# Kernel tuning notes

Measured on AMD Instinct MI355X. Metric: run time of the kernel, lower is better.

Reference implementation:

```python
import jax, jax.numpy as jnp
import numpy as np

B, S, D, H, DFF = 4, 2048, 1024, 16, 4096
DK = D // H  # = d_v
NEG = -1e30  # stands in for float('-inf'); fully-masked rows zeroed explicitly


def setup_inputs() -> dict:
    key = jax.random.key(0)
    ks = jax.random.split(key, 12)
    scale = lambda fan_in: fan_in ** -0.5
    # padding mask: positions >= random length are padded (True = pad)
    lens = jax.random.randint(ks[0], (B,), S // 2, S + 1)
    src_padding_mask = jnp.arange(S)[None, :] >= lens[:, None]
    return {
        "src": jax.random.normal(ks[1], (B, S, D), jnp.float32),
        "src_padding_mask": src_padding_mask,
        # per-head projections, stored as [H, D, DK] (x @ W, i.e. torch W.T)
        "Wq": jax.random.normal(ks[2], (H, D, DK), jnp.float32) * scale(D),
        "Wk": jax.random.normal(ks[3], (H, D, DK), jnp.float32) * scale(D),
        "Wv": jax.random.normal(ks[4], (H, D, DK), jnp.float32) * scale(D),
        "Wo": jax.random.normal(ks[5], (D, D), jnp.float32) * scale(D),
        "g1": jnp.ones((D,), jnp.float32),
        "g2": jnp.ones((D,), jnp.float32),
        "W1": jax.random.normal(ks[6], (D, DFF), jnp.float32) * scale(D),
        "V1": jax.random.normal(ks[7], (D, DFF), jnp.float32) * scale(D),
        "W2": jax.random.normal(ks[8], (DFF, D), jnp.float32) * scale(DFF),
    }


def _rmsnorm(x, gamma):
    # rms = sqrt(sum(x^2)/size); out = gamma * x / rms
    rms = jnp.sqrt(jnp.sum(x * x, axis=-1, keepdims=True) / x.shape[-1])
    return gamma * x / rms


def _encoder_layer(src, pad_mask, Wq, Wk, Wv, Wo, g1, g2, W1, V1, W2):
    x = _rmsnorm(src, g1)
    # all heads at once: q,k,v -> [B,H,S,DK]
    q = jnp.einsum('bsd,hdk->bhsk', x, Wq)
    k = jnp.einsum('bsd,hdk->bhsk', x, Wk)
    v = jnp.einsum('bsd,hdk->bhsk', x, Wv)
    scores = jnp.einsum('bhsk,bhtk->bhst', q, k) * (DK ** -0.5)  # [B,H,S,S]
    mask = pad_mask[:, None, :, None] | pad_mask[:, None, None, :]
    scores = jnp.where(mask, NEG, scores)
    attn = jax.nn.softmax(scores, axis=-1)
    # torch: fully -inf rows softmax to nan -> nan_to_num(0). Zero padded query rows.
    attn = jnp.where(pad_mask[:, None, :, None], 0.0, attn)
    o = jnp.einsum('bhst,bhtk->bhsk', attn, v)            # [B,H,S,DK]
    o = o.transpose(0, 2, 1, 3).reshape(src.shape[0], src.shape[1], -1)  # concat heads
    sa = src + o @ Wo
    y = _rmsnorm(sa, g2)
    ff = (jax.nn.silu(y @ W1) * (y @ V1)) @ W2
    return sa + ff


def reference(src, src_padding_mask, Wq, Wk, Wv, Wo, g1, g2, W1, V1, W2):
    return _encoder_layer(src, src_padding_mask, Wq, Wk, Wv, Wo, g1, g2, W1, V1, W2)
```

## Files before the change

kernel.cpp:

```cpp
#include <hip/hip_runtime.h>
#include <hip/hip_bf16.h>

typedef short short8 __attribute__((ext_vector_type(8)));
typedef float f32x4 __attribute__((ext_vector_type(4)));
typedef float f32x16 __attribute__((ext_vector_type(16)));
typedef unsigned short u16;
typedef unsigned short u16x4 __attribute__((ext_vector_type(4)));

__device__ __forceinline__ u16 f2bf(float f) {
  __hip_bfloat16 h = __float2bfloat16(f);
  return __builtin_bit_cast(u16, h);
}
__device__ __forceinline__ float bf2f(u16 u) {
  return __bfloat162float(__builtin_bit_cast(__hip_bfloat16, u));
}
__device__ __forceinline__ void gload_lds16(const void* g, void* l) {
  __builtin_amdgcn_global_load_lds(
      (const __attribute__((address_space(1))) void*)g,
      (__attribute__((address_space(3))) void*)l, 16, 0, 0);
}
__device__ __forceinline__ unsigned cvtpk(float lo, float hi) {
  unsigned r;
  asm("v_cvt_pk_bf16_f32 %0, %1, %2" : "=v"(r) : "v"(lo), "v"(hi));
  return r;
}

__global__ void compute_lens(const unsigned char* __restrict__ mask, int* __restrict__ lens) {
  __shared__ int flag;
  __shared__ int cnt[4];
  const int tid = threadIdx.x;
  if (tid == 0) flag = 0;
  if (tid < 4) cnt[tid] = 0;
  __syncthreads();
  int found = 0;
  for (int i = tid; i < 8192; i += 256)
    if (mask[i] == 1 && (i & 3) != 0) found = 1;
  if (found) atomicOr(&flag, 1);
  __syncthreads();
  int l0 = 0, l1 = 0, l2 = 0, l3 = 0;
  if (flag) {
    for (int i = tid; i < 8192; i += 256) {
      int z = (mask[i] == 0);
      int b = i >> 11;
      l0 += z & (b == 0); l1 += z & (b == 1); l2 += z & (b == 2); l3 += z & (b == 3);
    }
  } else {
    const int* mi = (const int*)mask;
    for (int i = tid; i < 8192; i += 256) {
      int z = (mi[i] == 0);
      int b = i >> 11;
      l0 += z & (b == 0); l1 += z & (b == 1); l2 += z & (b == 2); l3 += z & (b == 3);
    }
  }
  if (l0) atomicAdd(&cnt[0], l0);
  if (l1) atomicAdd(&cnt[1], l1);
  if (l2) atomicAdd(&cnt[2], l2);
  if (l3) atomicAdd(&cnt[3], l3);
  __syncthreads();
  if (tid < 4) lens[tid] = cnt[tid];
}

__global__ void convT_all(const float* __restrict__ Wq, const float* __restrict__ Wk,
                          const float* __restrict__ Wv, const float* __restrict__ Wo,
                          const float* __restrict__ W1, const float* __restrict__ V1,
                          const float* __restrict__ W2,
                          u16* __restrict__ WqkvT, u16* __restrict__ WoT,
                          u16* __restrict__ W1V1T, u16* __restrict__ W2T) {
  __shared__ float t[32][33];
  int b = (int)blockIdx.x;
  const float* in;
  u16* op;
  int K, N, n0, k0, ilv = 0;
  if (b < 3072) {
    const int which = b >> 10;
    b &= 1023;
    in = (which == 0) ? Wq : (which == 1) ? Wk : Wv;
    const int z = b >> 6;
    in += (size_t)z * 65536;
    op = WqkvT + (size_t)which * 1048576 + (size_t)z * 65536;
    K = 1024; N = 64;
    n0 = (b & 1) * 32; k0 = ((b >> 1) & 31) * 32;
  } else if (b < 4096) {
    b -= 3072;
    in = Wo; op = WoT; K = 1024; N = 1024;
    n0 = (b & 31) * 32; k0 = (b >> 5) * 32;
  } else if (b < 12288) {
    const int which = (b - 4096) >> 12;
    b = (b - 4096) & 4095;
    in = which ? V1 : W1; op = W1V1T; K = 1024; N = 4096; ilv = 1 + which;
    n0 = (b & 127) * 32; k0 = (b >> 7) * 32;
  } else {
    b -= 12288;
    in = W2; op = W2T; K = 4096; N = 1024;
    n0 = (b & 31) * 32; k0 = (b >> 5) * 32;
  }
  const int tx = threadIdx.x & 31, ty = threadIdx.x >> 5;
  for (int i = ty; i < 32; i += 8)
    t[i][tx] = in[(size_t)(k0 + i) * N + n0 + tx];
  __syncthreads();
  for (int i = ty; i < 32; i += 8) {
    const int rn = n0 + i;
    const int r = ilv ? ((((rn >> 4) << 5) | (rn & 15)) | ((ilv - 1) << 4)) : rn;
    op[(size_t)r * K + k0 + tx] = f2bf(t[tx][i]);
  }
}

__global__ void rmsnorm_kernel(const float* __restrict__ in, const float* __restrict__ g,
                               u16* __restrict__ out) {
  __shared__ float psum[4];
  const int row = blockIdx.x, tid = threadIdx.x;
  const float4 x = ((const float4*)(in + (size_t)row * 1024))[tid];
  float ss = x.x * x.x + x.y * x.y + x.z * x.z + x.w * x.w;
  for (int m = 1; m < 64; m <<= 1) ss += __shfl_xor(ss, m, 64);
  if ((tid & 63) == 0) psum[tid >> 6] = ss;
  __syncthreads();
  const float tot = psum[0] + psum[1] + psum[2] + psum[3];
  const float inv = rsqrtf(tot * (1.0f / 1024.0f));
  const float4 gv = ((const float4*)g)[tid];
  u16x4 o;
  o[0] = f2bf(gv.x * x.x * inv); o[1] = f2bf(gv.y * x.y * inv);
  o[2] = f2bf(gv.z * x.z * inv); o[3] = f2bf(gv.w * x.w * inv);
  *(u16x4*)&out[(size_t)row * 1024 + tid * 4] = o;
}

enum { MQKV = 0, MSA = 1, MFSILU = 2, MFF2 = 3 };

template <int MODE, int BM>
__global__ __launch_bounds__(512, (BM == 64) ? 4 : 2) void gemm3(
    const u16* __restrict__ A, const u16* __restrict__ Bt,
    const int K,
    u16* __restrict__ oq, u16* __restrict__ ok, u16* __restrict__ ov,
    float* __restrict__ of, const float* __restrict__ afp,
    u16* __restrict__ ob) {
  constexpr int ABUF = BM * 64;
  constexpr bool P4 = (BM == 256);
  constexpr int MR = BM / 32;
  constexpr int AIT = BM / 64;
  constexpr int AFR = (MR < 4) ? MR : 4;
  __shared__ u16 lds[2 * ABUF + 32768];
  const int tid = threadIdx.x;
  const int w = tid >> 6, l = tid & 63;
  const int wr = w >> 2, wc = w & 3;
  const int lane16 = l & 15, lgrp = l >> 4;

  const int bid = (int)blockIdx.x, xcd = bid & 7, seq = bid >> 3;
  int by, bx;
  if (MODE == MQKV) {
    const int j = seq / 24, t5 = seq % 24;
    by = (xcd >> 2) * 32 + j * 8 + t5 / 3;
    bx = (xcd & 3) * 3 + t5 % 3;
  } else if (MODE == MFSILU) {
    by = (seq >> 5) * 8 + ((seq & 31) >> 2);
    bx = xcd * 4 + (seq & 3);
  } else {
    by = (xcd >> 1) * 32 + (seq >> 1);
    bx = (xcd & 1) * 2 + (seq & 1);
  }
  const int row0 = by * BM, col0 = bx * 256;

  auto stageA = [&](int kt, int buf) {
#pragma unroll
    for (int i = 0; i < AIT; ++i) {
      const int cc = i * 512 + tid;
      const int r = cc >> 3, j = (cc & 7) ^ (r & 7);
      gload_lds16(A + (size_t)(row0 + r) * K + kt * 64 + j * 8,
                  &lds[buf * ABUF + cc * 8]);
    }
  };
  auto stageB = [&](int kt, int buf) {
#pragma unroll
    for (int i = 0; i < 4; ++i) {
      const int cc = i * 512 + tid;
      const int r = cc >> 3, j = (cc & 7) ^ (r & 7);
      gload_lds16(Bt + (size_t)(col0 + r) * K + kt * 64 + j * 8,
                  &lds[2 * ABUF + buf * 16384 + cc * 8]);
    }
  };
  auto frofs = [&](int rrow, int ks) {
    return rrow * 64 + ((((ks << 2) + lgrp) ^ (rrow & 7)) << 3);
  };

  f32x4 zero = {0.f, 0.f, 0.f, 0.f};
  f32x4 acc[MR][4];
#pragma unroll
  for (int i = 0; i < MR; ++i)
#pragma unroll
    for (int j = 0; j < 4; ++j) acc[i][j] = zero;

  const int nkt = K >> 6;
  stageA(0, 0); stageB(0, 0); stageA(1, 1);
  if (P4) stageB(1, 1);

  for (int t = 0; t < nkt; ++t) {
    const int c = t & 1;
    if (t == nkt - 1)       asm volatile("s_waitcnt vmcnt(0)\ns_barrier" ::: "memory");
    else if (P4)            asm volatile("s_waitcnt vmcnt(8)\ns_barrier" ::: "memory");
    else if (AIT == 2)      asm volatile("s_waitcnt vmcnt(2)\ns_barrier" ::: "memory");
    else                    asm volatile("s_waitcnt vmcnt(1)\ns_barrier" ::: "memory");
    const u16* ap = &lds[c * ABUF];
    const u16* bp = &lds[2 * ABUF + c * 16384];
    short8 a[AFR][2], b01[2][2], b23[2][2];

    if (!P4) { if (t + 1 < nkt) stageB(t + 1, c ^ 1); }
#pragma unroll
    for (int mi = 0; mi < AFR; ++mi)
#pragma unroll
      for (int ks = 0; ks < 2; ++ks)
        a[mi][ks] = *(const short8*)&ap[frofs(wr * (BM / 2) + mi * 16 + lane16, ks)];
#pragma unroll
    for (int ni = 0; ni < 2; ++ni)
#pragma unroll
      for (int ks = 0; ks < 2; ++ks) {
        b01[ni][ks] = *(const short8*)&bp[frofs(wc * 64 + ni * 16 + lane16, ks)];
        b23[ni][ks] = *(const short8*)&bp[frofs(wc * 64 + (ni + 2) * 16 + lane16, ks)];
      }
    __builtin_amdgcn_s_setprio(1);
#pragma unroll
    for (int ks = 0; ks < 2; ++ks)
#pragma unroll
      for (int mi = 0; mi < AFR; ++mi)
#pragma unroll
        for (int ni = 0; ni < 2; ++ni)
          acc[mi][ni] = __builtin_amdgcn_mfma_f32_16x16x32_bf16(a[mi][ks], b01[ni][ks], acc[mi][ni], 0, 0, 0);
    __builtin_amdgcn_s_setprio(0);
    asm volatile("s_barrier" ::: "memory");

    if (P4) {
      __builtin_amdgcn_s_setprio(1);
#pragma unroll
      for (int ks = 0; ks < 2; ++ks)
#pragma unroll
        for (int mi = 0; mi < 4; ++mi)
#pragma unroll
          for (int ni = 0; ni < 2; ++ni)
            acc[mi][ni + 2] = __builtin_amdgcn_mfma_f32_16x16x32_bf16(a[mi][ks], b23[ni][ks], acc[mi][ni + 2], 0, 0, 0);
      __builtin_amdgcn_s_setprio(0);
#pragma unroll
      for (int mi = 0; mi < 4; ++mi)
#pragma unroll
        for (int ks = 0; ks < 2; ++ks)
          a[mi][ks] = *(const short8*)&ap[frofs(wr * 128 + (mi + 4) * 16 + lane16, ks)];
      asm volatile("s_barrier" ::: "memory");

      if (t + 2 < nkt) stageB(t + 2, c);
      __builtin_amdgcn_s_setprio(1);
#pragma unroll
      for (int ks = 0; ks < 2; ++ks)
#pragma unroll
        for (int mi = 0; mi < 4; ++mi)
#pragma unroll
          for (int ni = 0; ni < 2; ++ni)
            acc[(MR == 8 ? mi + 4 : mi)][ni] = __builtin_amdgcn_mfma_f32_16x16x32_bf16(a[mi][ks], b01[ni][ks], acc[(MR == 8 ? mi + 4 : mi)][ni], 0, 0, 0);
      __builtin_amdgcn_s_setprio(0);
      asm volatile("s_barrier" ::: "memory");

      if (t + 2 < nkt) stageA(t + 2, c);
      __builtin_amdgcn_s_setprio(1);
#pragma unroll
      for (int ks = 0; ks < 2; ++ks)
#pragma unroll
        for (int mi = 0; mi < 4; ++mi)
#pragma unroll
          for (int ni = 0; ni < 2; ++ni)
            acc[(MR == 8 ? mi + 4 : mi)][ni + 2] = __builtin_amdgcn_mfma_f32_16x16x32_bf16(a[mi][ks], b23[ni][ks], acc[(MR == 8 ? mi + 4 : mi)][ni + 2], 0, 0, 0);
      __builtin_amdgcn_s_setprio(0);
    } else {
      if (t + 2 < nkt) stageA(t + 2, c);
      __builtin_amdgcn_s_setprio(1);
#pragma unroll
      for (int ks = 0; ks < 2; ++ks)
#pragma unroll
        for (int mi = 0; mi < AFR; ++mi)
#pragma unroll
          for (int ni = 0; ni < 2; ++ni)
            acc[mi][ni + 2] = __builtin_amdgcn_mfma_f32_16x16x32_bf16(a[mi][ks], b23[ni][ks], acc[mi][ni + 2], 0, 0, 0);
      __builtin_amdgcn_s_setprio(0);
    }
  }
  asm volatile("s_barrier" ::: "memory");

  if (MODE == MQKV) {
#pragma unroll
    for (int mi = 0; mi < MR; ++mi) {
      const int sbase = row0 + wr * (BM / 2) + mi * 16 + lgrp * 4;
      const int bbt = sbase >> 11, sr = sbase & 2047;
#pragma unroll
      for (int ni = 0; ni < 4; ++ni) {
        const int j = col0 + wc * 64 + ni * 16 + lane16;
        const int which = j >> 10, rr = j & 1023, h = rr >> 6, kk = rr & 63;
        const int bh = bbt * 16 + h;
        if (which == 2) {
          u16x4 pk;
#pragma unroll
          for (int r = 0; r < 4; ++r) pk[r] = f2bf(acc[mi][ni][r]);
          *(u16x4*)&ov[((size_t)bh * 64 + kk) * 2048 + sr] = pk;
        } else {
          u16* dst = (which == 0) ? oq : ok;
          const float scl = (which == 0) ? 0.125f : 1.0f;
#pragma unroll
          for (int r = 0; r < 4; ++r)
            dst[((size_t)bh * 2048 + sr + r) * 64 + kk] = f2bf(acc[mi][ni][r] * scl);
        }
      }
    }
  } else if (MODE == MFSILU) {
    u16* ep = &lds[w * 576];
    const int orow = l >> 2, ocol = (l & 3) * 8;
#pragma unroll
    for (int mi = 0; mi < MR; ++mi) {
#pragma unroll
      for (int p = 0; p < 2; ++p)
#pragma unroll
        for (int r = 0; r < 4; ++r) {
          const float h1 = acc[mi][2 * p][r], h2 = acc[mi][2 * p + 1][r];
          ep[(lgrp * 4 + r) * 34 + p * 16 + lane16] = f2bf(h1 / (1.0f + __expf(-h1)) * h2);
        }
      short8 v = *(const short8*)&ep[orow * 34 + ocol];
      *(short8*)&ob[(size_t)(row0 + wr * (BM / 2) + mi * 16 + orow) * 4096 +
                    (col0 >> 1) + wc * 32 + ocol] = v;
    }
  } else {
#pragma unroll
    for (int mi = 0; mi < MR; ++mi) {
      const int row = row0 + wr * (BM / 2) + mi * 16 + lgrp * 4;
#pragma unroll
      for (int ni = 0; ni < 4; ++ni) {
        const int j = col0 + wc * 64 + ni * 16 + lane16;
#pragma unroll
        for (int r = 0; r < 4; ++r) {
          const size_t idx = (size_t)(row + r) * 1024 + j;
          const float base = (MODE == MSA) ? afp[idx] : of[idx];
          of[idx] = base + acc[mi][ni][r];
        }
      }
    }
  }
}

__global__ void attn2_kernel(const u16* __restrict__ qb, const u16* __restrict__ kb,
                             const u16* __restrict__ vT, u16* __restrict__ obuf,
                             const int* __restrict__ lens) {
  __shared__ u16 sm[9216];
  const int tid = threadIdx.x;
  const int l = tid & 63, wid = tid >> 6;
  const int l31 = l & 31, hi = l >> 5;
  const int bh = blockIdx.x, b = bh >> 4, h = bh & 15;
  const int q0 = blockIdx.y * 128;
  const int len = lens[b];

  if (q0 >= len) {
    short8 z = {0, 0, 0, 0, 0, 0, 0, 0};
#pragma unroll
    for (int c = 0; c < 4; ++c) {
      const int ck = c * 256 + tid;
      const int r = ck >> 3, j = ck & 7;
      *(short8*)&obuf[((size_t)b * 2048 + q0 + r) * 1024 + h * 64 + j * 8] = z;
    }
    return;
  }

  const int q0w = q0 + wid * 32;
  const u16* qp = qb + ((size_t)bh * 2048 + q0w + l31) * 64;
  short8 qf0 = *(const short8*)(qp + hi * 8);
  short8 qf1 = *(const short8*)(qp + 16 + hi * 8);
  short8 qf2 = *(const short8*)(qp + 32 + hi * 8);
  short8 qf3 = *(const short8*)(qp + 48 + hi * 8);

  f32x16 oa0 = {0.f,0.f,0.f,0.f,0.f,0.f,0.f,0.f,0.f,0.f,0.f,0.f,0.f,0.f,0.f,0.f};
  f32x16 oa1 = oa0;
  float m_run = -1e30f, l_run = 0.f;

  const int swz = (l31 & 7) << 3;
  const int nt = (len + 63) >> 6;
  for (int kt = 0; kt < nt; ++kt) {
    const int t0 = kt * 64;
    __syncthreads();
#pragma unroll
    for (int c = 0; c < 2; ++c) {
      const int ck = c * 256 + wid * 64 + l;
      const int r = ck >> 3;
      const int j = (ck & 7) ^ (r & 7);
      gload_lds16(kb + ((size_t)bh * 2048 + t0 + r) * 64 + j * 8,
                  &sm[(c * 256 + wid * 64) * 8]);
      gload_lds16(vT + ((size_t)bh * 64 + r) * 2048 + t0 + j * 8,
                  &sm[4096 + (c * 256 + wid * 64) * 8]);
    }
    __syncthreads();

    f32x16 sc0 = {0.f,0.f,0.f,0.f,0.f,0.f,0.f,0.f,0.f,0.f,0.f,0.f,0.f,0.f,0.f,0.f};
    f32x16 sc1 = sc0;
#pragma unroll
    for (int ds = 0; ds < 4; ++ds) {
      const int col = (ds * 16 + hi * 8) ^ swz;
      const short8 kf0 = *(const short8*)&sm[(0 + l31) * 64 + col];
      const short8 kf1 = *(const short8*)&sm[(32 + l31) * 64 + col];
      const short8 qf = (ds == 0) ? qf0 : (ds == 1) ? qf1 : (ds == 2) ? qf2 : qf3;
      sc0 = __builtin_amdgcn_mfma_f32_32x32x16_bf16(kf0, qf, sc0, 0, 0, 0);
      sc1 = __builtin_amdgcn_mfma_f32_32x32x16_bf16(kf1, qf, sc1, 0, 0, 0);
    }

    if (t0 + 64 > len) {
      const int tb = t0 + 4 * hi;
#pragma unroll
      for (int i = 0; i < 16; ++i) {
        const int tg = tb + (i & 3) + 8 * (i >> 2);
        if (tg >= len) sc0[i] = -1e30f;
        if (tg + 32 >= len) sc1[i] = -1e30f;
      }
    }

    float mt = sc0[0];
#pragma unroll
    for (int i = 1; i < 16; ++i) mt = fmaxf(mt, sc0[i]);
#pragma unroll
    for (int i = 0; i < 16; ++i) mt = fmaxf(mt, sc1[i]);
    mt = fmaxf(mt, __shfl_xor(mt, 32, 64));
    const float mnew = fmaxf(m_run, mt);
    const float fac = __expf(m_run - mnew);
    m_run = mnew;
    float sum = 0.f;
#pragma unroll
    for (int i = 0; i < 16; ++i) { sc0[i] = __expf(sc0[i] - mnew); sum += sc0[i]; }
#pragma unroll
    for (int i = 0; i < 16; ++i) { sc1[i] = __expf(sc1[i] - mnew); sum += sc1[i]; }
    sum += __shfl_xor(sum, 32, 64);
    l_run = l_run * fac + sum;
#pragma unroll
    for (int i = 0; i < 16; ++i) { oa0[i] *= fac; oa1[i] *= fac; }

    unsigned wv[16];
#pragma unroll
    for (int k = 0; k < 8; ++k) wv[k] = cvtpk(sc0[2 * k], sc0[2 * k + 1]);
#pragma unroll
    for (int k = 0; k < 8; ++k) wv[8 + k] = cvtpk(sc1[2 * k], sc1[2 * k + 1]);
    unsigned pw[16];
#pragma unroll
    for (int s = 0; s < 2; ++s) {
#pragma unroll
      for (int half = 0; half < 2; ++half) {
        const unsigned a0 = wv[8 * s + 4 * half + 0], a1 = wv[8 * s + 4 * half + 1];
        const unsigned a2 = wv[8 * s + 4 * half + 2], a3 = wv[8 * s + 4 * half + 3];
        const unsigned e0 = (unsigned)__shfl_xor((int)(hi ? a0 : a2), 32, 64);
        const unsigned e1 = (unsigned)__shfl_xor((int)(hi ? a1 : a3), 32, 64);
        const int o = s * 8 + half * 4;
        pw[o + 0] = hi ? e0 : a0;
        pw[o + 1] = hi ? e1 : a1;
        pw[o + 2] = hi ? a2 : e0;
        pw[o + 3] = hi ? a3 : e1;
      }
    }
#pragma unroll
    for (int g = 0; g < 4; ++g) {
      union { unsigned u[4]; short8 s8; } pk;
      pk.u[0] = pw[4 * g + 0]; pk.u[1] = pw[4 * g + 1];
      pk.u[2] = pw[4 * g + 2]; pk.u[3] = pw[4 * g + 3];
      const int col = (g * 16 + hi * 8) ^ swz;
      const short8 vf0 = *(const short8*)&sm[4096 + (0 + l31) * 64 + col];
      const short8 vf1 = *(const short8*)&sm[4096 + (32 + l31) * 64 + col];
      oa0 = __builtin_amdgcn_mfma_f32_32x32x16_bf16(vf0, pk.s8, oa0, 0, 0, 0);
      oa1 = __builtin_amdgcn_mfma_f32_32x32x16_bf16(vf1, pk.s8, oa1, 0, 0, 0);
    }
  }

  __syncthreads();
  const float invl = 1.0f / l_run;
  u16* ow = &sm[wid * 2304];
#pragma unroll
  for (int i = 0; i < 16; ++i) {
    const int d0 = (i & 3) + 8 * (i >> 2) + 4 * hi;
    ow[l31 * 72 + d0] = f2bf(oa0[i] * invl);
    ow[l31 * 72 + 32 + d0] = f2bf(oa1[i] * invl);
  }
  short8 z = {0, 0, 0, 0, 0, 0, 0, 0};
#pragma unroll
  for (int c = 0; c < 4; ++c) {
    const int ck = c * 64 + l;
    const int r = ck >> 3, j = ck & 7;
    short8 v = *(const short8*)&ow[r * 72 + j * 8];
    if (q0w + r >= len) v = z;
    *(short8*)&obuf[((size_t)b * 2048 + q0w + r) * 1024 + h * 64 + j * 8] = v;
  }
}

extern "C" void kernel_launch(void* const* d_in, const int* in_sizes, int n_in,
                              void* d_out, int out_size, void* d_ws, size_t ws_size,
                              hipStream_t stream) {
  const float* src = (const float*)d_in[0];
  const unsigned char* mask = (const unsigned char*)d_in[1];
  const float* Wq = (const float*)d_in[2];
  const float* Wk = (const float*)d_in[3];
  const float* Wv = (const float*)d_in[4];
  const float* Wo = (const float*)d_in[5];
  const float* g1 = (const float*)d_in[6];
  const float* g2 = (const float*)d_in[7];
  const float* W1 = (const float*)d_in[8];
  const float* V1 = (const float*)d_in[9];
  const float* W2 = (const float*)d_in[10];
  float* out = (float*)d_out;
  char* ws = (char*)d_ws;

  int* lens   = (int*)ws;
  u16* WqkvT  = (u16*)(ws + 256);
  u16* WoT    = (u16*)(ws + 6291712);
  u16* W1V1T  = (u16*)(ws + 8388864);
  u16* W2T    = (u16*)(ws + 25166080);
  u16* xb     = (u16*)(ws + 33554688);
  u16* qbf    = (u16*)(ws + 50331904);
  u16* kbf    = (u16*)(ws + 67109120);
  u16* vTb    = (u16*)(ws + 83886336);
  u16* obf    = (u16*)(ws + 100663552);
  u16* c1     = qbf;

  compute_lens<<<1, 256, 0, stream>>>(mask, lens);
  convT_all<<<16384, 256, 0, stream>>>(Wq, Wk, Wv, Wo, W1, V1, W2,
                                       WqkvT, WoT, W1V1T, W2T);

  rmsnorm_kernel<<<8192, 256, 0, stream>>>(src, g1, xb);
  gemm3<MQKV, 128><<<768, 512, 0, stream>>>(xb, WqkvT, 1024,
                                            qbf, kbf, vTb, nullptr, nullptr, nullptr);
  attn2_kernel<<<dim3(64, 16), 256, 0, stream>>>(qbf, kbf, vTb, obf, lens);
  gemm3<MSA, 64><<<512, 512, 0, stream>>>(obf, WoT, 1024,
                                          nullptr, nullptr, nullptr, out, src, nullptr);
  rmsnorm_kernel<<<8192, 256, 0, stream>>>(out, g2, xb);
  gemm3<MFSILU, 256><<<1024, 512, 0, stream>>>(xb, W1V1T, 1024,
                                               nullptr, nullptr, nullptr, nullptr, nullptr, c1);
  gemm3<MFF2, 64><<<512, 512, 0, stream>>>(c1, W2T, 4096,
                                           nullptr, nullptr, nullptr, out, nullptr, nullptr);
}
```

Baseline: 447.6 us.

## Switch GEMMs to 32x32x16 MFMA tiles and fuse prep kernels into one launch

Rewrites the GEMM inner loop to use 32x32x16 bf16 MFMA instructions with 16-element accumulators instead of 16x16x32. This cuts the number of MFMA issues and LDS fragment reads per tile. It also changes the W1/V1 interleave to 32-column groups to match the new tile, and rewrites the epilogues for the 32x32 output layout. Separately, it merges the length computation, weight transpose/convert and first RMSNorm into a single prep kernel to save launch overhead. The risks are higher register pressure from the larger accumulators and different LDS bank behaviour in the epilogue.

```diff
diff --git a/kernel.cpp b/kernel.cpp
--- a/kernel.cpp
+++ b/kernel.cpp
@@ -2,7 +2,6 @@
 #include <hip/hip_bf16.h>
 
 typedef short short8 __attribute__((ext_vector_type(8)));
-typedef float f32x4 __attribute__((ext_vector_type(4)));
 typedef float f32x16 __attribute__((ext_vector_type(16)));
 typedef unsigned short u16;
 typedef unsigned short u16x4 __attribute__((ext_vector_type(4)));
@@ -25,49 +24,71 @@
   return r;
 }
 
-__global__ void compute_lens(const unsigned char* __restrict__ mask, int* __restrict__ lens) {
+__global__ void prep_kernel(const unsigned char* __restrict__ mask,
+                            const float* __restrict__ src, const float* __restrict__ g1,
+                            const float* __restrict__ Wq, const float* __restrict__ Wk,
+                            const float* __restrict__ Wv, const float* __restrict__ Wo,
+                            const float* __restrict__ W1, const float* __restrict__ V1,
+                            const float* __restrict__ W2,
+                            int* __restrict__ lens, u16* __restrict__ WqkvT,
+                            u16* __restrict__ WoT, u16* __restrict__ W1V1T,
+                            u16* __restrict__ W2T, u16* __restrict__ xb) {
+  __shared__ float t[32][33];
+  __shared__ float psum[4];
   __shared__ int flag;
   __shared__ int cnt[4];
+  int b = (int)blockIdx.x;
   const int tid = threadIdx.x;
-  if (tid == 0) flag = 0;
-  if (tid < 4) cnt[tid] = 0;
-  __syncthreads();
-  int found = 0;
-  for (int i = tid; i < 8192; i += 256)
-    if (mask[i] == 1 && (i & 3) != 0) found = 1;
-  if (found) atomicOr(&flag, 1);
-  __syncthreads();
-  int l0 = 0, l1 = 0, l2 = 0, l3 = 0;
-  if (flag) {
-    for (int i = tid; i < 8192; i += 256) {
-      int z = (mask[i] == 0);
-      int b = i >> 11;
-      l0 += z & (b == 0); l1 += z & (b == 1); l2 += z & (b == 2); l3 += z & (b == 3);
-    }
-  } else {
-    const int* mi = (const int*)mask;
-    for (int i = tid; i < 8192; i += 256) {
-      int z = (mi[i] == 0);
-      int b = i >> 11;
-      l0 += z & (b == 0); l1 += z & (b == 1); l2 += z & (b == 2); l3 += z & (b == 3);
-    }
-  }
-  if (l0) atomicAdd(&cnt[0], l0);
-  if (l1) atomicAdd(&cnt[1], l1);
-  if (l2) atomicAdd(&cnt[2], l2);
-  if (l3) atomicAdd(&cnt[3], l3);
-  __syncthreads();
-  if (tid < 4) lens[tid] = cnt[tid];
-}
-
-__global__ void convT_all(const float* __restrict__ Wq, const float* __restrict__ Wk,
-                          const float* __restrict__ Wv, const float* __restrict__ Wo,
-                          const float* __restrict__ W1, const float* __restrict__ V1,
-                          const float* __restrict__ W2,
-                          u16* __restrict__ WqkvT, u16* __restrict__ WoT,
-                          u16* __restrict__ W1V1T, u16* __restrict__ W2T) {
-  __shared__ float t[32][33];
-  int b = (int)blockIdx.x;
+
+  if (b >= 16384) {
+    if (b == 24576) {
+      if (tid == 0) flag = 0;
+      if (tid < 4) cnt[tid] = 0;
+      __syncthreads();
+      int found = 0;
+      for (int i = tid; i < 8192; i += 256)
+        if (mask[i] == 1 && (i & 3) != 0) found = 1;
+      if (found) atomicOr(&flag, 1);
+      __syncthreads();
+      int l0 = 0, l1 = 0, l2 = 0, l3 = 0;
+      if (flag) {
+        for (int i = tid; i < 8192; i += 256) {
+          int z = (mask[i] == 0);
+          int bb = i >> 11;
+          l0 += z & (bb == 0); l1 += z & (bb == 1); l2 += z & (bb == 2); l3 += z & (bb == 3);
+        }
+      } else {
+        const int* mi = (const int*)mask;
+        for (int i = tid; i < 8192; i += 256) {
+          int z = (mi[i] == 0);
+          int bb = i >> 11;
+          l0 += z & (bb == 0); l1 += z & (bb == 1); l2 += z & (bb == 2); l3 += z & (bb == 3);
+        }
+      }
+      if (l0) atomicAdd(&cnt[0], l0);
+      if (l1) atomicAdd(&cnt[1], l1);
+      if (l2) atomicAdd(&cnt[2], l2);
+      if (l3) atomicAdd(&cnt[3], l3);
+      __syncthreads();
+      if (tid < 4) lens[tid] = cnt[tid];
+    } else {
+      const int row = b - 16384;
+      const float4 x = ((const float4*)(src + (size_t)row * 1024))[tid];
+      float ss = x.x * x.x + x.y * x.y + x.z * x.z + x.w * x.w;
+      for (int m = 1; m < 64; m <<= 1) ss += __shfl_xor(ss, m, 64);
+      if ((tid & 63) == 0) psum[tid >> 6] = ss;
+      __syncthreads();
+      const float tot = psum[0] + psum[1] + psum[2] + psum[3];
+      const float inv = rsqrtf(tot * (1.0f / 1024.0f));
+      const float4 gv = ((const float4*)g1)[tid];
+      u16x4 o;
+      o[0] = f2bf(gv.x * x.x * inv); o[1] = f2bf(gv.y * x.y * inv);
+      o[2] = f2bf(gv.z * x.z * inv); o[3] = f2bf(gv.w * x.w * inv);
+      *(u16x4*)&xb[(size_t)row * 1024 + tid * 4] = o;
+    }
+    return;
+  }
+
   const float* in;
   u16* op;
   int K, N, n0, k0, ilv = 0;
@@ -94,13 +115,13 @@
     in = W2; op = W2T; K = 4096; N = 1024;
     n0 = (b & 31) * 32; k0 = (b >> 5) * 32;
   }
-  const int tx = threadIdx.x & 31, ty = threadIdx.x >> 5;
+  const int tx = tid & 31, ty = tid >> 5;
   for (int i = ty; i < 32; i += 8)
     t[i][tx] = in[(size_t)(k0 + i) * N + n0 + tx];
   __syncthreads();
   for (int i = ty; i < 32; i += 8) {
     const int rn = n0 + i;
-    const int r = ilv ? ((((rn >> 4) << 5) | (rn & 15)) | ((ilv - 1) << 4)) : rn;
+    const int r = ilv ? ((rn >> 5) * 64 + (ilv - 1) * 32 + (rn & 31)) : rn;
     op[(size_t)r * K + k0 + tx] = f2bf(t[tx][i]);
   }
 }
@@ -126,7 +147,7 @@
 enum { MQKV = 0, MSA = 1, MFSILU = 2, MFF2 = 3 };
 
 template <int MODE, int BM>
-__global__ __launch_bounds__(512, (BM == 64) ? 4 : 2) void gemm3(
+__global__ __launch_bounds__(512, (BM == 64) ? 4 : 2) void gemm5(
     const u16* __restrict__ A, const u16* __restrict__ Bt,
     const int K,
     u16* __restrict__ oq, u16* __restrict__ ok, u16* __restrict__ ov,
@@ -134,14 +155,14 @@
     u16* __restrict__ ob) {
   constexpr int ABUF = BM * 64;
   constexpr bool P4 = (BM == 256);
-  constexpr int MR = BM / 32;
+  constexpr int MB = BM / 64;
   constexpr int AIT = BM / 64;
-  constexpr int AFR = (MR < 4) ? MR : 4;
+  constexpr int AH = P4 ? 2 : MB;
   __shared__ u16 lds[2 * ABUF + 32768];
   const int tid = threadIdx.x;
   const int w = tid >> 6, l = tid & 63;
   const int wr = w >> 2, wc = w & 3;
-  const int lane16 = l & 15, lgrp = l >> 4;
+  const int l31 = l & 31, hi = l >> 5;
 
   const int bid = (int)blockIdx.x, xcd = bid & 7, seq = bid >> 3;
   int by, bx;
@@ -176,16 +197,19 @@
                   &lds[2 * ABUF + buf * 16384 + cc * 8]);
     }
   };
-  auto frofs = [&](int rrow, int ks) {
-    return rrow * 64 + ((((ks << 2) + lgrp) ^ (rrow & 7)) << 3);
+  auto frofs = [&](int rbase, int ks16) {
+    const int rrow = rbase + l31;
+    const int chunk = ((ks16 << 1) + hi) ^ (rrow & 7);
+    return rrow * 64 + chunk * 8;
   };
 
-  f32x4 zero = {0.f, 0.f, 0.f, 0.f};
-  f32x4 acc[MR][4];
-#pragma unroll
-  for (int i = 0; i < MR; ++i)
-#pragma unroll
-    for (int j = 0; j < 4; ++j) acc[i][j] = zero;
+  f32x16 acc[MB][2];
+#pragma unroll
+  for (int i = 0; i < MB; ++i)
+#pragma unroll
+    for (int j = 0; j < 2; ++j)
+#pragma unroll
+      for (int k = 0; k < 16; ++k) acc[i][j][k] = 0.f;
 
   const int nkt = K >> 6;
   stageA(0, 0); stageB(0, 0); stageA(1, 1);
@@ -199,81 +223,69 @@
     else                    asm volatile("s_waitcnt vmcnt(1)\ns_barrier" ::: "memory");
     const u16* ap = &lds[c * ABUF];
     const u16* bp = &lds[2 * ABUF + c * 16384];
-    short8 a[AFR][2], b01[2][2], b23[2][2];
+    short8 a[AH][4], b0[4], b1[4];
 
     if (!P4) { if (t + 1 < nkt) stageB(t + 1, c ^ 1); }
 #pragma unroll
-    for (int mi = 0; mi < AFR; ++mi)
-#pragma unroll
-      for (int ks = 0; ks < 2; ++ks)
-        a[mi][ks] = *(const short8*)&ap[frofs(wr * (BM / 2) + mi * 16 + lane16, ks)];
-#pragma unroll
-    for (int ni = 0; ni < 2; ++ni)
-#pragma unroll
-      for (int ks = 0; ks < 2; ++ks) {
-        b01[ni][ks] = *(const short8*)&bp[frofs(wc * 64 + ni * 16 + lane16, ks)];
-        b23[ni][ks] = *(const short8*)&bp[frofs(wc * 64 + (ni + 2) * 16 + lane16, ks)];
-      }
+    for (int mi = 0; mi < AH; ++mi)
+#pragma unroll
+      for (int ks = 0; ks < 4; ++ks)
+        a[mi][ks] = *(const short8*)&ap[frofs(wr * (BM / 2) + mi * 32, ks)];
+#pragma unroll
+    for (int ks = 0; ks < 4; ++ks) {
+      b0[ks] = *(const short8*)&bp[frofs(wc * 64, ks)];
+      b1[ks] = *(const short8*)&bp[frofs(wc * 64 + 32, ks)];
+    }
     __builtin_amdgcn_s_setprio(1);
 #pragma unroll
-    for (int ks = 0; ks < 2; ++ks)
-#pragma unroll
-      for (int mi = 0; mi < AFR; ++mi)
-#pragma unroll
-        for (int ni = 0; ni < 2; ++ni)
-          acc[mi][ni] = __builtin_amdgcn_mfma_f32_16x16x32_bf16(a[mi][ks], b01[ni][ks], acc[mi][ni], 0, 0, 0);
+    for (int ks = 0; ks < 4; ++ks)
+#pragma unroll
+      for (int mi = 0; mi < AH; ++mi)
+        acc[mi][0] = __builtin_amdgcn_mfma_f32_32x32x16_bf16(a[mi][ks], b0[ks], acc[mi][0], 0, 0, 0);
     __builtin_amdgcn_s_setprio(0);
     asm volatile("s_barrier" ::: "memory");
 
     if (P4) {
       __builtin_amdgcn_s_setprio(1);
 #pragma unroll
-      for (int ks = 0; ks < 2; ++ks)
-#pragma unroll
-        for (int mi = 0; mi < 4; ++mi)
-#pragma unroll
-          for (int ni = 0; ni < 2; ++ni)
-            acc[mi][ni + 2] = __builtin_amdgcn_mfma_f32_16x16x32_bf16(a[mi][ks], b23[ni][ks], acc[mi][ni + 2], 0, 0, 0);
+      for (int ks = 0; ks < 4; ++ks)
+#pragma unroll
+        for (int mi = 0; mi < 2; ++mi)
+          acc[mi][1] = __builtin_amdgcn_mfma_f32_32x32x16_bf16(a[mi][ks], b1[ks], acc[mi][1], 0, 0, 0);
       __builtin_amdgcn_s_setprio(0);
 #pragma unroll
-      for (int mi = 0; mi < 4; ++mi)
-#pragma unroll
-        for (int ks = 0; ks < 2; ++ks)
-          a[mi][ks] = *(const short8*)&ap[frofs(wr * 128 + (mi + 4) * 16 + lane16, ks)];
+      for (int mi = 0; mi < 2; ++mi)
+#pragma unroll
+        for (int ks = 0; ks < 4; ++ks)
+          a[mi][ks] = *(const short8*)&ap[frofs(wr * 128 + (mi + 2) * 32, ks)];
       asm volatile("s_barrier" ::: "memory");
 
       if (t + 2 < nkt) stageB(t + 2, c);
       __builtin_amdgcn_s_setprio(1);
 #pragma unroll
-      for (int ks = 0; ks < 2; ++ks)
-#pragma unroll
-        for (int mi = 0; mi < 4; ++mi)
-#pragma unroll
-          for (int ni = 0; ni < 2; ++ni)
-            acc[(MR == 8 ? mi + 4 : mi)][ni] = __builtin_amdgcn_mfma_f32_16x16x32_bf16(a[mi][ks], b01[ni][ks], acc[(MR == 8 ? mi + 4 : mi)][ni], 0, 0, 0);
+      for (int ks = 0; ks < 4; ++ks)
+#pragma unroll
+        for (int mi = 0; mi < 2; ++mi)
+          acc[(MB == 4 ? mi + 2 : mi)][0] = __builtin_amdgcn_mfma_f32_32x32x16_bf16(a[mi][ks], b0[ks], acc[(MB == 4 ? mi + 2 : mi)][0], 0, 0, 0);
       __builtin_amdgcn_s_setprio(0);
       asm volatile("s_barrier" ::: "memory");
 
       if (t + 2 < nkt) stageA(t + 2, c);
       __builtin_amdgcn_s_setprio(1);
 #pragma unroll
-      for (int ks = 0; ks < 2; ++ks)
-#pragma unroll
-        for (int mi = 0; mi < 4; ++mi)
-#pragma unroll
-          for (int ni = 0; ni < 2; ++ni)
-            acc[(MR == 8 ? mi + 4 : mi)][ni + 2] = __builtin_amdgcn_mfma_f32_16x16x32_bf16(a[mi][ks], b23[ni][ks], acc[(MR == 8 ? mi + 4 : mi)][ni + 2], 0, 0, 0);
+      for (int ks = 0; ks < 4; ++ks)
+#pragma unroll
+        for (int mi = 0; mi < 2; ++mi)
+          acc[(MB == 4 ? mi + 2 : mi)][1] = __builtin_amdgcn_mfma_f32_32x32x16_bf16(a[mi][ks], b1[ks], acc[(MB == 4 ? mi + 2 : mi)][1], 0, 0, 0);
       __builtin_amdgcn_s_setprio(0);
     } else {
       if (t + 2 < nkt) stageA(t + 2, c);
       __builtin_amdgcn_s_setprio(1);
 #pragma unroll
-      for (int ks = 0; ks < 2; ++ks)
-#pragma unroll
-        for (int mi = 0; mi < AFR; ++mi)
-#pragma unroll
-          for (int ni = 0; ni < 2; ++ni)
-            acc[mi][ni + 2] = __builtin_amdgcn_mfma_f32_16x16x32_bf16(a[mi][ks], b23[ni][ks], acc[mi][ni + 2], 0, 0, 0);
+      for (int ks = 0; ks < 4; ++ks)
+#pragma unroll
+        for (int mi = 0; mi < AH; ++mi)
+          acc[mi][1] = __builtin_amdgcn_mfma_f32_32x32x16_bf16(a[mi][ks], b1[ks], acc[mi][1], 0, 0, 0);
       __builtin_amdgcn_s_setprio(0);
     }
   }
@@ -281,56 +293,65 @@
 
   if (MODE == MQKV) {
 #pragma unroll
-    for (int mi = 0; mi < MR; ++mi) {
-      const int sbase = row0 + wr * (BM / 2) + mi * 16 + lgrp * 4;
-      const int bbt = sbase >> 11, sr = sbase & 2047;
-#pragma unroll
-      for (int ni = 0; ni < 4; ++ni) {
-        const int j = col0 + wc * 64 + ni * 16 + lane16;
+    for (int mi = 0; mi < MB; ++mi) {
+      const int sbase = row0 + wr * (BM / 2) + mi * 32 + 4 * hi;
+#pragma unroll
+      for (int ni = 0; ni < 2; ++ni) {
+        const int j = col0 + wc * 64 + ni * 32 + l31;
         const int which = j >> 10, rr = j & 1023, h = rr >> 6, kk = rr & 63;
+        const int bbt = sbase >> 11, sr = sbase & 2047;
         const int bh = bbt * 16 + h;
         if (which == 2) {
-          u16x4 pk;
-#pragma unroll
-          for (int r = 0; r < 4; ++r) pk[r] = f2bf(acc[mi][ni][r]);
-          *(u16x4*)&ov[((size_t)bh * 64 + kk) * 2048 + sr] = pk;
+#pragma unroll
+          for (int q = 0; q < 4; ++q) {
+            u16x4 pk;
+#pragma unroll
+            for (int r = 0; r < 4; ++r) pk[r] = f2bf(acc[mi][ni][4 * q + r]);
+            *(u16x4*)&ov[((size_t)bh * 64 + kk) * 2048 + sr + 8 * q] = pk;
+          }
         } else {
           u16* dst = (which == 0) ? oq : ok;
           const float scl = (which == 0) ? 0.125f : 1.0f;
 #pragma unroll
-          for (int r = 0; r < 4; ++r)
-            dst[((size_t)bh * 2048 + sr + r) * 64 + kk] = f2bf(acc[mi][ni][r] * scl);
+          for (int reg = 0; reg < 16; ++reg) {
+            const int s = sr + (reg & 3) + 8 * (reg >> 2);
+            dst[((size_t)bh * 2048 + s) * 64 + kk] = f2bf(acc[mi][ni][reg] * scl);
+          }
         }
       }
     }
   } else if (MODE == MFSILU) {
-    u16* ep = &lds[w * 576];
-    const int orow = l >> 2, ocol = (l & 3) * 8;
-#pragma unroll
-    for (int mi = 0; mi < MR; ++mi) {
-#pragma unroll
-      for (int p = 0; p < 2; ++p)
-#pragma unroll
-        for (int r = 0; r < 4; ++r) {
-          const float h1 = acc[mi][2 * p][r], h2 = acc[mi][2 * p + 1][r];
-          ep[(lgrp * 4 + r) * 34 + p * 16 + lane16] = f2bf(h1 / (1.0f + __expf(-h1)) * h2);
-        }
-      short8 v = *(const short8*)&ep[orow * 34 + ocol];
-      *(short8*)&ob[(size_t)(row0 + wr * (BM / 2) + mi * 16 + orow) * 4096 +
-                    (col0 >> 1) + wc * 32 + ocol] = v;
+    u16* ep = &lds[w * 1280];
+    const int ocol = (col0 >> 1) + wc * 32;
+#pragma unroll
+    for (int mi = 0; mi < MB; ++mi) {
+#pragma unroll
+      for (int reg = 0; reg < 16; ++reg) {
+        const float h1 = acc[mi][0][reg], h2 = acc[mi][1][reg];
+        const int rrow = (reg & 3) + 8 * (reg >> 2) + 4 * hi;
+        ep[rrow * 36 + l31] = f2bf(h1 / (1.0f + __expf(-h1)) * h2);
+      }
+#pragma unroll
+      for (int cch = 0; cch < 2; ++cch) {
+        const int ck = cch * 64 + l;
+        const int r2 = ck >> 2, jj = (ck & 3) * 8;
+        short8 v = *(const short8*)&ep[r2 * 36 + jj];
+        *(short8*)&ob[(size_t)(row0 + wr * 128 + mi * 32 + r2) * 4096 + ocol + jj] = v;
+      }
     }
   } else {
 #pragma unroll
-    for (int mi = 0; mi < MR; ++mi) {
-      const int row = row0 + wr * (BM / 2) + mi * 16 + lgrp * 4;
-#pragma unroll
-      for (int ni = 0; ni < 4; ++ni) {
-        const int j = col0 + wc * 64 + ni * 16 + lane16;
-#pragma unroll
-        for (int r = 0; r < 4; ++r) {
-          const size_t idx = (size_t)(row + r) * 1024 + j;
+    for (int mi = 0; mi < MB; ++mi) {
+      const int rbase = row0 + wr * (BM / 2) + mi * 32 + 4 * hi;
+#pragma unroll
+      for (int ni = 0; ni < 2; ++ni) {
+        const int j = col0 + wc * 64 + ni * 32 + l31;
+#pragma unroll
+        for (int reg = 0; reg < 16; ++reg) {
+          const int row = rbase + (reg & 3) + 8 * (reg >> 2);
+          const size_t idx = (size_t)row * 1024 + j;
           const float base = (MODE == MSA) ? afp[idx] : of[idx];
-          of[idx] = base + acc[mi][ni][r];
+          of[idx] = base + acc[mi][ni][reg];
         }
       }
     }
@@ -511,19 +532,16 @@
   u16* obf    = (u16*)(ws + 100663552);
   u16* c1     = qbf;
 
-  compute_lens<<<1, 256, 0, stream>>>(mask, lens);
-  convT_all<<<16384, 256, 0, stream>>>(Wq, Wk, Wv, Wo, W1, V1, W2,
-                                       WqkvT, WoT, W1V1T, W2T);
-
-  rmsnorm_kernel<<<8192, 256, 0, stream>>>(src, g1, xb);
-  gemm3<MQKV, 128><<<768, 512, 0, stream>>>(xb, WqkvT, 1024,
+  prep_kernel<<<24577, 256, 0, stream>>>(mask, src, g1, Wq, Wk, Wv, Wo, W1, V1, W2,
+                                         lens, WqkvT, WoT, W1V1T, W2T, xb);
+  gemm5<MQKV, 128><<<768, 512, 0, stream>>>(xb, WqkvT, 1024,
                                             qbf, kbf, vTb, nullptr, nullptr, nullptr);
   attn2_kernel<<<dim3(64, 16), 256, 0, stream>>>(qbf, kbf, vTb, obf, lens);
-  gemm3<MSA, 64><<<512, 512, 0, stream>>>(obf, WoT, 1024,
+  gemm5<MSA, 64><<<512, 512, 0, stream>>>(obf, WoT, 1024,
                                           nullptr, nullptr, nullptr, out, src, nullptr);
   rmsnorm_kernel<<<8192, 256, 0, stream>>>(out, g2, xb);
-  gemm3<MFSILU, 256><<<1024, 512, 0, stream>>>(xb, W1V1T, 1024,
+  gemm5<MFSILU, 256><<<1024, 512, 0, stream>>>(xb, W1V1T, 1024,
                                                nullptr, nullptr, nullptr, nullptr, nullptr, c1);
-  gemm3<MFF2, 64><<<512, 512, 0, stream>>>(c1, W2T, 4096,
+  gemm5<MFF2, 64><<<512, 512, 0, stream>>>(c1, W2T, 4096,
                                            nullptr, nullptr, nullptr, out, nullptr, nullptr);
 }
```

After: 491.2 us. 1.1x slower.
